# Optimization experiments

Measured on AMD Instinct MI355X. Metric: run time of the kernel, lower is better.

Reference implementation:

```python
import jax, jax.numpy as jnp
import numpy as np

VOCAB = 50257
D_MODEL = 1024
PAD_IDX = 0
B, L = 4, 4096


def setup_inputs() -> dict:
    key = jax.random.key(0)
    k_emb, k_R, k_ids, k_role = jax.random.split(key, 4)
    emb = jax.random.normal(k_emb, (VOCAB, D_MODEL), dtype=jnp.float32)
    emb = emb.at[PAD_IDX].set(0.0)  # nn.Embedding padding_idx row is zero
    R = jax.random.normal(k_R, (D_MODEL, D_MODEL), dtype=jnp.float32)
    input_ids = jax.random.randint(k_ids, (B, L), 0, VOCAB, dtype=jnp.int64)
    role_mask = jax.random.randint(k_role, (B, L), 0, 2, dtype=jnp.int64)
    return {"input_ids": input_ids, "role_mask": role_mask, "emb": emb, "R": R}


def reference(input_ids, role_mask, emb, R):
    # embedding gather: (B, L, D)
    x = emb[input_ids]
    # agent tokens get x @ R.T, user tokens pass through
    agent = (role_mask == 1)[..., None]
    transformed = jnp.einsum('bld,ed->ble', x, R)
    return jnp.where(agent, transformed, x)
```

## Files before the change

kernel.cpp:

```cpp
#include <hip/hip_runtime.h>
#include <hip/hip_bf16.h>
#include <stdint.h>

#define DMODEL 1024
#define M_TOK  16384

typedef __attribute__((ext_vector_type(8))) short short8;
typedef __attribute__((ext_vector_type(4))) float f32x4;

__device__ __forceinline__ unsigned int pack2_bf16(float f0, float f1) {
    unsigned int u0 = __builtin_bit_cast(unsigned int, f0);
    unsigned int u1 = __builtin_bit_cast(unsigned int, f1);
    u0 += 0x7fffu + ((u0 >> 16) & 1u);
    u1 += 0x7fffu + ((u1 >> 16) & 1u);
    return __builtin_amdgcn_perm(u1, u0, 0x07060302);
}

__device__ __forceinline__ void gload_lds16(const void* g, void* l) {
    __builtin_amdgcn_global_load_lds(
        (const __attribute__((address_space(1))) void*)g,
        (__attribute__((address_space(3))) void*)l, 16, 0, 0);
}

__global__ void gather_convert(const int* __restrict__ ids,
                               const float* __restrict__ emb,
                               const float* __restrict__ Rm,
                               __hip_bfloat16* __restrict__ Xb,
                               __hip_bfloat16* __restrict__ Rb) {
    const int row  = blockIdx.x * 4 + (threadIdx.x >> 6);
    const int lane = threadIdx.x & 63;
    const float* src;
    __hip_bfloat16* dst;
    if (row < M_TOK) {
        src = emb + (size_t)ids[row] * DMODEL;
        dst = Xb + (size_t)row * DMODEL;
    } else {
        src = Rm + (size_t)(row - M_TOK) * DMODEL;
        dst = Rb + (size_t)(row - M_TOK) * DMODEL;
    }
#pragma unroll
    for (int c = 0; c < 4; ++c) {
        const int idx = c * 256 + lane * 4;
        float4 v = *(const float4*)(src + idx);
        uint2 p = make_uint2(pack2_bf16(v.x, v.y), pack2_bf16(v.z, v.w));
        *(uint2*)((unsigned short*)dst + idx) = p;
    }
}

__global__ void rse_gemm2(const int* __restrict__ roles,
                          const __hip_bfloat16* __restrict__ Xb,
                          const __hip_bfloat16* __restrict__ Rb,
                          float* __restrict__ out) {
    __shared__ __hip_bfloat16 As[128 * 32];
    __shared__ __hip_bfloat16 Bs[128 * 32];
    __shared__ int s_role[128];

    const int tid  = threadIdx.x;
    const int m0   = blockIdx.y * 128;
    const int n0   = blockIdx.x * 128;
    const int lane = tid & 63;
    const int wave = tid >> 6;
    const int quad = lane >> 4;
    const int l15  = lane & 15;
    const int wr   = wave >> 1;
    const int wc   = wave & 1;

    if (tid < 128) s_role[tid] = roles[m0 + tid];

    const int st_row = lane >> 2;
    const int st_k   = (lane & 3) * 8;
    const int rg0 = wave * 16;
    const int rg1 = (4 + wave) * 16;

    const __hip_bfloat16* aG = Xb + (size_t)m0 * DMODEL;
    const __hip_bfloat16* bG = Rb + (size_t)n0 * DMODEL;

    f32x4 acc[4][4] = {};

    for (int k0 = 0; k0 < DMODEL; k0 += 32) {
        __syncthreads();
        gload_lds16(aG + (size_t)(rg0 + st_row) * DMODEL + k0 + st_k, &As[rg0 * 32]);
        gload_lds16(aG + (size_t)(rg1 + st_row) * DMODEL + k0 + st_k, &As[rg1 * 32]);
        gload_lds16(bG + (size_t)(rg0 + st_row) * DMODEL + k0 + st_k, &Bs[rg0 * 32]);
        gload_lds16(bG + (size_t)(rg1 + st_row) * DMODEL + k0 + st_k, &Bs[rg1 * 32]);
        __syncthreads();

        short8 af[4], bfr[4];
#pragma unroll
        for (int i = 0; i < 4; ++i)
            af[i] = *(const short8*)&As[(wr * 64 + i * 16 + l15) * 32 + quad * 8];
#pragma unroll
        for (int j = 0; j < 4; ++j)
            bfr[j] = *(const short8*)&Bs[(wc * 64 + j * 16 + l15) * 32 + quad * 8];
#pragma unroll
        for (int i = 0; i < 4; ++i)
#pragma unroll
            for (int j = 0; j < 4; ++j)
                acc[i][j] = __builtin_amdgcn_mfma_f32_16x16x32_bf16(af[i], bfr[j], acc[i][j], 0, 0, 0);
    }

    const int colbase = n0 + wc * 64 + l15;
#pragma unroll
    for (int ti = 0; ti < 4; ++ti) {
        const int rowb = wr * 64 + ti * 16 + quad * 4;
#pragma unroll
        for (int r = 0; r < 4; ++r) {
            const int row  = rowb + r;
            const int role = s_role[row];
            const __hip_bfloat16* src = Xb + (size_t)(m0 + row) * DMODEL + colbase;
            float* dst = out + (size_t)(m0 + row) * DMODEL + colbase;
#pragma unroll
            for (int tj = 0; tj < 4; ++tj) {
                float v = acc[ti][tj][r];
                if (!role) v = (float)src[tj * 16];
                dst[tj * 16] = v;
            }
        }
    }
}

extern "C" void kernel_launch(void* const* d_in, const int* in_sizes, int n_in,
                              void* d_out, int out_size, void* d_ws, size_t ws_size,
                              hipStream_t stream) {
    const int*   ids   = (const int*)d_in[0];
    const int*   roles = (const int*)d_in[1];
    const float* emb   = (const float*)d_in[2];
    const float* Rm    = (const float*)d_in[3];
    float*       out   = (float*)d_out;

    __hip_bfloat16* Xb = (__hip_bfloat16*)d_ws;
    __hip_bfloat16* Rb = Xb + (size_t)M_TOK * DMODEL;

    gather_convert<<<(M_TOK + DMODEL) / 4, 256, 0, stream>>>(ids, emb, Rm, Xb, Rb);

    dim3 grid2(DMODEL / 128, M_TOK / 128);
    rse_gemm2<<<grid2, 256, 0, stream>>>(roles, Xb, Rb, out);
}
```

Measured before the change: 329.0 us.

## Compact agent tokens and run the GEMM only over agent rows

Adds a single-block prefix-scan kernel that compacts agent-role token indices, so the gather writes bf16 rows only for agent tokens and copies user-token rows straight to the output in fp32. The GEMM then runs over the compacted agent rows only, with early exit for tiles past the agent count, and scatters results back through the index map. This targets the roughly half of the matmul work spent on user tokens, and also removes the bf16 round-trip for passthrough rows, which improves their accuracy. In exchange it adds a serial single-block scan launch, an indirect scatter on store, and a grid whose later blocks exit immediately.

```diff
diff --git a/kernel.cpp b/kernel.cpp
--- a/kernel.cpp
+++ b/kernel.cpp
@@ -22,42 +22,95 @@
         (__attribute__((address_space(3))) void*)l, 16, 0, 0);
 }
 
-__global__ void gather_convert(const int* __restrict__ ids,
-                               const float* __restrict__ emb,
-                               const float* __restrict__ Rm,
-                               __hip_bfloat16* __restrict__ Xb,
-                               __hip_bfloat16* __restrict__ Rb) {
+__global__ void plan_compact(const int* __restrict__ roles,
+                             int* __restrict__ pos, int* __restrict__ orig,
+                             int* __restrict__ n_agent) {
+    __shared__ int s[1024];
+    const int t = threadIdx.x;
+    int pred[16];
+    int c = 0;
+#pragma unroll
+    for (int i = 0; i < 16; ++i) {
+        pred[i] = (roles[i * 1024 + t] == 1);
+        c += pred[i];
+    }
+    s[t] = c;
+    __syncthreads();
+    for (int off = 1; off < 1024; off <<= 1) {
+        int v = (t >= off) ? s[t - off] : 0;
+        __syncthreads();
+        s[t] += v;
+        __syncthreads();
+    }
+    int base = s[t] - c;
+#pragma unroll
+    for (int i = 0; i < 16; ++i) {
+        if (pred[i]) {
+            const int m = i * 1024 + t;
+            orig[base] = m;
+            pos[m] = base;
+            ++base;
+        }
+    }
+    if (t == 1023) *n_agent = s[1023];
+}
+
+__global__ void gather2(const int* __restrict__ ids, const int* __restrict__ roles,
+                        const int* __restrict__ pos,
+                        const float* __restrict__ emb, const float* __restrict__ Rm,
+                        __hip_bfloat16* __restrict__ Xc,
+                        __hip_bfloat16* __restrict__ Rb,
+                        float* __restrict__ out) {
     const int row  = blockIdx.x * 4 + (threadIdx.x >> 6);
     const int lane = threadIdx.x & 63;
-    const float* src;
-    __hip_bfloat16* dst;
     if (row < M_TOK) {
-        src = emb + (size_t)ids[row] * DMODEL;
-        dst = Xb + (size_t)row * DMODEL;
+        const float* src = emb + (size_t)ids[row] * DMODEL;
+        if (roles[row] == 1) {
+            __hip_bfloat16* dst = Xc + (size_t)pos[row] * DMODEL;
+#pragma unroll
+            for (int c = 0; c < 4; ++c) {
+                const int idx = c * 256 + lane * 4;
+                float4 v = *(const float4*)(src + idx);
+                uint2 p = make_uint2(pack2_bf16(v.x, v.y), pack2_bf16(v.z, v.w));
+                *(uint2*)((unsigned short*)dst + idx) = p;
+            }
+        } else {
+            float* dst = out + (size_t)row * DMODEL;
+#pragma unroll
+            for (int c = 0; c < 4; ++c) {
+                const int idx = c * 256 + lane * 4;
+                *(float4*)(dst + idx) = *(const float4*)(src + idx);
+            }
+        }
     } else {
-        src = Rm + (size_t)(row - M_TOK) * DMODEL;
-        dst = Rb + (size_t)(row - M_TOK) * DMODEL;
-    }
+        const int r = row - M_TOK;
+        const float* src = Rm + (size_t)r * DMODEL;
+        __hip_bfloat16* dst = Rb + (size_t)r * DMODEL;
 #pragma unroll
-    for (int c = 0; c < 4; ++c) {
-        const int idx = c * 256 + lane * 4;
-        float4 v = *(const float4*)(src + idx);
-        uint2 p = make_uint2(pack2_bf16(v.x, v.y), pack2_bf16(v.z, v.w));
-        *(uint2*)((unsigned short*)dst + idx) = p;
+        for (int c = 0; c < 4; ++c) {
+            const int idx = c * 256 + lane * 4;
+            float4 v = *(const float4*)(src + idx);
+            uint2 p = make_uint2(pack2_bf16(v.x, v.y), pack2_bf16(v.z, v.w));
+            *(uint2*)((unsigned short*)dst + idx) = p;
+        }
     }
 }
 
-__global__ void rse_gemm2(const int* __restrict__ roles,
-                          const __hip_bfloat16* __restrict__ Xb,
+__global__ void rse_gemm3(const int* __restrict__ n_agent_p,
+                          const int* __restrict__ orig,
+                          const __hip_bfloat16* __restrict__ Xc,
                           const __hip_bfloat16* __restrict__ Rb,
                           float* __restrict__ out) {
+    const int na = *n_agent_p;
+    const int m0 = blockIdx.x * 128;
+    if (m0 >= na) return;
+    const int n0 = blockIdx.y * 128;
+
     __shared__ __hip_bfloat16 As[128 * 32];
     __shared__ __hip_bfloat16 Bs[128 * 32];
-    __shared__ int s_role[128];
+    __shared__ int s_orig[128];
 
     const int tid  = threadIdx.x;
-    const int m0   = blockIdx.y * 128;
-    const int n0   = blockIdx.x * 128;
     const int lane = tid & 63;
     const int wave = tid >> 6;
     const int quad = lane >> 4;
@@ -65,14 +118,17 @@
     const int wr   = wave >> 1;
     const int wc   = wave & 1;
 
-    if (tid < 128) s_role[tid] = roles[m0 + tid];
+    if (tid < 128) {
+        const int j = m0 + tid;
+        s_orig[tid] = (j < na) ? orig[j] : -1;
+    }
 
     const int st_row = lane >> 2;
     const int st_k   = (lane & 3) * 8;
     const int rg0 = wave * 16;
     const int rg1 = (4 + wave) * 16;
 
-    const __hip_bfloat16* aG = Xb + (size_t)m0 * DMODEL;
+    const __hip_bfloat16* aG = Xc + (size_t)m0 * DMODEL;
     const __hip_bfloat16* bG = Rb + (size_t)n0 * DMODEL;
 
     f32x4 acc[4][4] = {};
@@ -105,15 +161,13 @@
         const int rowb = wr * 64 + ti * 16 + quad * 4;
 #pragma unroll
         for (int r = 0; r < 4; ++r) {
-            const int row  = rowb + r;
-            const int role = s_role[row];
-            const __hip_bfloat16* src = Xb + (size_t)(m0 + row) * DMODEL + colbase;
-            float* dst = out + (size_t)(m0 + row) * DMODEL + colbase;
+            const int row = rowb + r;
+            const int oj  = s_orig[row];
+            if (oj >= 0) {
+                float* dst = out + (size_t)oj * DMODEL + colbase;
 #pragma unroll
-            for (int tj = 0; tj < 4; ++tj) {
-                float v = acc[ti][tj][r];
-                if (!role) v = (float)src[tj * 16];
-                dst[tj * 16] = v;
+                for (int tj = 0; tj < 4; ++tj)
+                    dst[tj * 16] = acc[ti][tj][r];
             }
         }
     }
@@ -128,11 +182,14 @@
     const float* Rm    = (const float*)d_in[3];
     float*       out   = (float*)d_out;
 
-    __hip_bfloat16* Xb = (__hip_bfloat16*)d_ws;
-    __hip_bfloat16* Rb = Xb + (size_t)M_TOK * DMODEL;
+    __hip_bfloat16* Xc = (__hip_bfloat16*)d_ws;
+    __hip_bfloat16* Rb = Xc + (size_t)M_TOK * DMODEL;
+    int* orig    = (int*)(Rb + (size_t)DMODEL * DMODEL);
+    int* pos     = orig + M_TOK;
+    int* n_agent = pos + M_TOK;
 
-    gather_convert<<<(M_TOK + DMODEL) / 4, 256, 0, stream>>>(ids, emb, Rm, Xb, Rb);
-
-    dim3 grid2(DMODEL / 128, M_TOK / 128);
-    rse_gemm2<<<grid2, 256, 0, stream>>>(roles, Xb, Rb, out);
+    plan_compact<<<1, 1024, 0, stream>>>(roles, pos, orig, n_agent);
+    gather2<<<(M_TOK + DMODEL) / 4, 256, 0, stream>>>(ids, roles, pos, emb, Rm, Xc, Rb, out);
+    dim3 grid2(M_TOK / 128, DMODEL / 128);
+    rse_gemm3<<<grid2, 256, 0, stream>>>(n_agent, orig, Xc, Rb, out);
 }
```

Result: faster. 318.1 us (-3.3%).

## Compact agent tokens and run GEMM only on them, fusing gather into GEMM

Applied to the files above, without the earlier changes.

A planning kernel compacts the indices of agent tokens with ballot and an atomic offset, and converts R to bf16. A fused kernel then runs the GEMM only over the compacted agent rows. It gathers embedding rows directly from fp32 and converts them to bf16 into LDS, and scatters results to their original positions. Extra blocks copy user-token rows straight from the embedding table. This roughly halves the GEMM work and removes the bf16 staging buffer for X. In exchange it adds a memset, an atomic-ordered compaction, and non-async A loads inside the K loop.

```diff
diff --git a/kernel.cpp b/kernel.cpp
--- a/kernel.cpp
+++ b/kernel.cpp
@@ -22,67 +22,121 @@
         (__attribute__((address_space(3))) void*)l, 16, 0, 0);
 }
 
-__global__ void gather_convert(const int* __restrict__ ids,
-                               const float* __restrict__ emb,
-                               const float* __restrict__ Rm,
-                               __hip_bfloat16* __restrict__ Xb,
-                               __hip_bfloat16* __restrict__ Rb) {
-    const int row  = blockIdx.x * 4 + (threadIdx.x >> 6);
-    const int lane = threadIdx.x & 63;
-    const float* src;
-    __hip_bfloat16* dst;
-    if (row < M_TOK) {
-        src = emb + (size_t)ids[row] * DMODEL;
-        dst = Xb + (size_t)row * DMODEL;
+__global__ void plan_kernel(const int* __restrict__ roles, const float* __restrict__ Rm,
+                            int* __restrict__ orig, int* __restrict__ n_agent,
+                            __hip_bfloat16* __restrict__ Rb) {
+    const int t = threadIdx.x;
+    if (blockIdx.x < 64) {
+        const int tok  = blockIdx.x * 256 + t;
+        const int pred = (roles[tok] == 1);
+        const int lane = t & 63;
+        const int wave = t >> 6;
+        unsigned long long b = __ballot(pred);
+        const int rank   = __popcll(b & ((1ull << lane) - 1ull));
+        const int wtotal = __popcll(b);
+        __shared__ int woff[4];
+        __shared__ int sbase;
+        if (lane == 0) woff[wave] = wtotal;
+        __syncthreads();
+        if (t == 0) {
+            int s0 = woff[0], s1 = woff[1], s2 = woff[2], s3 = woff[3];
+            sbase = atomicAdd(n_agent, s0 + s1 + s2 + s3);
+            woff[0] = 0; woff[1] = s0; woff[2] = s0 + s1; woff[3] = s0 + s1 + s2;
+        }
+        __syncthreads();
+        if (pred) orig[sbase + woff[wave] + rank] = tok;
     } else {
-        src = Rm + (size_t)(row - M_TOK) * DMODEL;
-        dst = Rb + (size_t)(row - M_TOK) * DMODEL;
-    }
-#pragma unroll
-    for (int c = 0; c < 4; ++c) {
-        const int idx = c * 256 + lane * 4;
-        float4 v = *(const float4*)(src + idx);
-        uint2 p = make_uint2(pack2_bf16(v.x, v.y), pack2_bf16(v.z, v.w));
-        *(uint2*)((unsigned short*)dst + idx) = p;
+        const int rblk = blockIdx.x - 64;
+        const size_t base = (size_t)rblk * 32 * DMODEL;
+        for (int s = 0; s < 32; ++s) {
+            const size_t idx = base + s * 1024 + t * 4;
+            float4 v = *(const float4*)(Rm + idx);
+            uint2 p = make_uint2(pack2_bf16(v.x, v.y), pack2_bf16(v.z, v.w));
+            *(uint2*)((unsigned short*)Rb + idx) = p;
+        }
     }
 }
 
-__global__ void rse_gemm2(const int* __restrict__ roles,
-                          const __hip_bfloat16* __restrict__ Xb,
-                          const __hip_bfloat16* __restrict__ Rb,
-                          float* __restrict__ out) {
+__global__ void mega(const int* __restrict__ ids, const int* __restrict__ roles,
+                     const float* __restrict__ emb, const __hip_bfloat16* __restrict__ Rb,
+                     const int* __restrict__ orig, const int* __restrict__ n_agent_p,
+                     float* __restrict__ out) {
     __shared__ __hip_bfloat16 As[128 * 32];
     __shared__ __hip_bfloat16 Bs[128 * 32];
-    __shared__ int s_role[128];
+    __shared__ int s_oj[128];
+    __shared__ int s_srow[128];
 
     const int tid  = threadIdx.x;
-    const int m0   = blockIdx.y * 128;
-    const int n0   = blockIdx.x * 128;
     const int lane = tid & 63;
     const int wave = tid >> 6;
+
+    if (blockIdx.x >= 1024) {
+        const int cb = blockIdx.x - 1024;
+#pragma unroll
+        for (int r = 0; r < 4; ++r) {
+            const int row = cb * 16 + wave * 4 + r;
+            if (roles[row] != 1) {
+                const float* src = emb + (size_t)ids[row] * DMODEL;
+                float* dst = out + (size_t)row * DMODEL;
+#pragma unroll
+                for (int c = 0; c < 4; ++c) {
+                    const int idx = c * 256 + lane * 4;
+                    *(float4*)(dst + idx) = *(const float4*)(src + idx);
+                }
+            }
+        }
+        return;
+    }
+
+    const int na = *n_agent_p;
+    const int mt = blockIdx.x & 127;
+    const int nt = blockIdx.x >> 7;
+    const int m0 = mt * 128;
+    if (m0 >= na) return;
+    const int n0 = nt * 128;
+
     const int quad = lane >> 4;
     const int l15  = lane & 15;
     const int wr   = wave >> 1;
     const int wc   = wave & 1;
 
-    if (tid < 128) s_role[tid] = roles[m0 + tid];
+    if (tid < 128) {
+        const int j  = m0 + tid;
+        const int oj = (j < na) ? orig[j] : -1;
+        s_oj[tid]   = oj;
+        s_srow[tid] = (oj >= 0) ? ids[oj] : 0;
+    }
+    __syncthreads();
+
+    const int sr = tid >> 1;
+    const int sh = tid & 1;
+    const float* aRow = emb + (size_t)s_srow[sr] * DMODEL + sh * 16;
 
     const int st_row = lane >> 2;
     const int st_k   = (lane & 3) * 8;
     const int rg0 = wave * 16;
     const int rg1 = (4 + wave) * 16;
-
-    const __hip_bfloat16* aG = Xb + (size_t)m0 * DMODEL;
     const __hip_bfloat16* bG = Rb + (size_t)n0 * DMODEL;
 
     f32x4 acc[4][4] = {};
 
     for (int k0 = 0; k0 < DMODEL; k0 += 32) {
+        float4 a0 = *(const float4*)(aRow + k0);
+        float4 a1 = *(const float4*)(aRow + k0 + 4);
+        float4 a2 = *(const float4*)(aRow + k0 + 8);
+        float4 a3 = *(const float4*)(aRow + k0 + 12);
+
         __syncthreads();
-        gload_lds16(aG + (size_t)(rg0 + st_row) * DMODEL + k0 + st_k, &As[rg0 * 32]);
-        gload_lds16(aG + (size_t)(rg1 + st_row) * DMODEL + k0 + st_k, &As[rg1 * 32]);
         gload_lds16(bG + (size_t)(rg0 + st_row) * DMODEL + k0 + st_k, &Bs[rg0 * 32]);
         gload_lds16(bG + (size_t)(rg1 + st_row) * DMODEL + k0 + st_k, &Bs[rg1 * 32]);
+
+        uint4 p0 = make_uint4(pack2_bf16(a0.x, a0.y), pack2_bf16(a0.z, a0.w),
+                              pack2_bf16(a1.x, a1.y), pack2_bf16(a1.z, a1.w));
+        uint4 p1 = make_uint4(pack2_bf16(a2.x, a2.y), pack2_bf16(a2.z, a2.w),
+                              pack2_bf16(a3.x, a3.y), pack2_bf16(a3.z, a3.w));
+        *(uint4*)&As[sr * 32 + sh * 16]     = p0;
+        *(uint4*)&As[sr * 32 + sh * 16 + 8] = p1;
+
         __syncthreads();
 
         short8 af[4], bfr[4];
@@ -105,15 +159,13 @@
         const int rowb = wr * 64 + ti * 16 + quad * 4;
 #pragma unroll
         for (int r = 0; r < 4; ++r) {
-            const int row  = rowb + r;
-            const int role = s_role[row];
-            const __hip_bfloat16* src = Xb + (size_t)(m0 + row) * DMODEL + colbase;
-            float* dst = out + (size_t)(m0 + row) * DMODEL + colbase;
+            const int row = rowb + r;
+            const int oj  = s_oj[row];
+            if (oj >= 0) {
+                float* dst = out + (size_t)oj * DMODEL + colbase;
 #pragma unroll
-            for (int tj = 0; tj < 4; ++tj) {
-                float v = acc[ti][tj][r];
-                if (!role) v = (float)src[tj * 16];
-                dst[tj * 16] = v;
+                for (int tj = 0; tj < 4; ++tj)
+                    dst[tj * 16] = acc[ti][tj][r];
             }
         }
     }
@@ -128,11 +180,11 @@
     const float* Rm    = (const float*)d_in[3];
     float*       out   = (float*)d_out;
 
-    __hip_bfloat16* Xb = (__hip_bfloat16*)d_ws;
-    __hip_bfloat16* Rb = Xb + (size_t)M_TOK * DMODEL;
+    __hip_bfloat16* Rb = (__hip_bfloat16*)d_ws;
+    int* orig    = (int*)(Rb + (size_t)DMODEL * DMODEL);
+    int* n_agent = orig + M_TOK;
 
-    gather_convert<<<(M_TOK + DMODEL) / 4, 256, 0, stream>>>(ids, emb, Rm, Xb, Rb);
-
-    dim3 grid2(DMODEL / 128, M_TOK / 128);
-    rse_gemm2<<<grid2, 256, 0, stream>>>(roles, Xb, Rb, out);
+    hipMemsetAsync(n_agent, 0, sizeof(int), stream);
+    plan_kernel<<<96, 256, 0, stream>>>(roles, Rm, orig, n_agent, Rb);
+    mega<<<2048, 256, 0, stream>>>(ids, roles, emb, Rb, orig, n_agent, out);
 }
```

New measurement: 329.1 us. About the same (+0.0%).
